# Optimization experiments

Measured on AMD Instinct MI355X. Metric: run time of the kernel, lower is better.

Reference implementation:

```python
import jax, jax.numpy as jnp
import numpy as np

B, H, S, D = 2, 16, 2048, 64

def setup_inputs() -> dict:
    key = jax.random.key(0)
    kq, kk, kv = jax.random.split(key, 3)
    query = jax.random.normal(kq, (B, H, S, D), dtype=jnp.float32)
    key_t = jax.random.normal(kk, (B, H, S, D), dtype=jnp.float32)
    value = jax.random.normal(kv, (B, H, S, D), dtype=jnp.float32)
    # causal mask, broadcast over heads; 0 => masked out
    mask = jnp.tril(jnp.ones((S, S), dtype=jnp.int32))[None, None, :, :]
    mask = jnp.broadcast_to(mask, (B, 1, S, S))
    return {"query": query, "key": key_t, "value": value, "mask": mask}

def reference(query, key, value, mask):
    d_k = query.shape[-1]
    scale = 1.0 / jnp.sqrt(jnp.float32(d_k))
    # [B,H,S,S] scores
    scores = jnp.einsum("bhqd,bhkd->bhqk", query, key) * scale
    scores = jnp.where(mask == 0, jnp.float32(-1e9), scores)
    attn_weights = jax.nn.softmax(scores, axis=-1)
    # dropout is identity in eval mode (reference baseline)
    context = jnp.einsum("bhqk,bhkd->bhqd", attn_weights, value)
    return context, attn_weights
```

## Files before the change

kernel.cpp:

```cpp
#include <hip/hip_runtime.h>

#define S_LEN 2048
#define D_DIM 64
#define BH_N  32
#define QT    64
#define NQT   (S_LEN / QT)
#define SWZ(r) (((r) & 7) << 4)

typedef short bf16x8 __attribute__((ext_vector_type(8)));
typedef float f32x4  __attribute__((ext_vector_type(4)));
typedef unsigned short u16;
typedef unsigned int   u32;

static __device__ __forceinline__ u16 f2bf(float x) {
    unsigned u = __float_as_uint(x);
    u += 0x7fffu + ((u >> 16) & 1u);
    return (u16)(u >> 16);
}
static __device__ __forceinline__ u32 pack2(float a, float b) {
    return (u32)f2bf(a) | ((u32)f2bf(b) << 16);
}

#define MFMA(a, b, acc) __builtin_amdgcn_mfma_f32_16x16x32_bf16((a), (b), (acc), 0, 0, 0)

static __device__ __forceinline__ void gld16(const void* g, void* l) {
    __builtin_amdgcn_global_load_lds((const __attribute__((address_space(1))) void*)g,
                                     (__attribute__((address_space(3))) void*)l, 16, 0, 0);
}

__global__ __launch_bounds__(256)
void build_imgs(const float* __restrict__ K, const float* __restrict__ V,
                u16* __restrict__ Kimg, u16* __restrict__ Vimg)
{
    const int blk = blockIdx.x;
    const int tid = threadIdx.x;
    const float* Ksrc = K + (size_t)blk * 4096;
    const float* Vsrc = V + (size_t)blk * 4096;
    char* Kt = (char*)(Kimg + (size_t)blk * 4096);
    char* Vt = (char*)(Vimg + (size_t)blk * 4096);
    {
        int kr = tid >> 2, kcb = (tid & 3) * 16;
        const float* p = Ksrc + kr * 64 + kcb;
        float4 a = ((const float4*)p)[0], b = ((const float4*)p)[1];
        float4 e = ((const float4*)p)[2], d = ((const float4*)p)[3];
        u32 t[8] = {pack2(a.x,a.y), pack2(a.z,a.w), pack2(b.x,b.y), pack2(b.z,b.w),
                    pack2(e.x,e.y), pack2(e.z,e.w), pack2(d.x,d.y), pack2(d.z,d.w)};
        char* dst = Kt + kr * 128;
        *(uint4*)(dst + ((2*kcb)      ^ SWZ(kr))) = ((uint4*)t)[0];
        *(uint4*)(dst + ((2*kcb + 16) ^ SWZ(kr))) = ((uint4*)t)[1];
    }
    {
        int vk2 = (tid & 31) * 2, vdh = tid >> 5;
        const float* p0 = Vsrc + vk2 * 64 + vdh * 8;
        const float* p1 = p0 + 64;
        float4 a0 = ((const float4*)p0)[0], b0 = ((const float4*)p0)[1];
        float4 a1 = ((const float4*)p1)[0], b1 = ((const float4*)p1)[1];
        float e0[8] = {a0.x,a0.y,a0.z,a0.w,b0.x,b0.y,b0.z,b0.w};
        float e1[8] = {a1.x,a1.y,a1.z,a1.w,b1.x,b1.y,b1.z,b1.w};
        #pragma unroll
        for (int i = 0; i < 8; ++i) {
            int d = vdh * 8 + i;
            *(u32*)(Vt + d * 128 + ((2 * vk2) ^ SWZ(d))) = pack2(e0[i], e1[i]);
        }
    }
}

__global__ __launch_bounds__(256, 4)
void sdpa_pipe(const float* __restrict__ Qg, const u16* __restrict__ Kimg,
               const u16* __restrict__ Vimg, float* __restrict__ out)
{
    __shared__ __attribute__((aligned(16))) char Ksh[2][8192];
    __shared__ __attribute__((aligned(16))) char Vsh[2][8192];
    __shared__ __attribute__((aligned(16))) char Ps[4 * 2048];

    const int tid  = threadIdx.x;
    const int lane = tid & 63;
    const int w    = tid >> 6;
    const int g    = lane >> 4;
    const int c    = lane & 15;

    const int b  = blockIdx.x;
    const int bh = b & (BH_N - 1);
    const int t  = b >> 5;
    const int ti = t & 7, tj = t >> 3;
    const int qi = (tj == 0) ? ti : (tj == 1) ? (15 - ti) : (tj == 2) ? (16 + ti) : (31 - ti);
    const int q0 = qi * QT;

    const char*  Kt = (const char*)(Kimg + (size_t)bh * 32 * 4096);
    const char*  Vt = (const char*)(Vimg + (size_t)bh * 32 * 4096);
    const float* Qh = Qg + (size_t)bh * S_LEN * D_DIM;
    float* ctx  = out + (size_t)bh * S_LEN * D_DIM;
    float* attn = out + (size_t)BH_N * S_LEN * D_DIM + (size_t)bh * S_LEN * S_LEN;

    const int qrow = q0 + w * 16 + c;

    bf16x8 qf0, qf1;
    {
        const float* qp = Qh + (size_t)qrow * D_DIM;
        #pragma unroll
        for (int h = 0; h < 2; ++h) {
            int d0 = h * 32 + g * 8;
            float4 x = *reinterpret_cast<const float4*>(qp + d0);
            float4 y = *reinterpret_cast<const float4*>(qp + d0 + 4);
            u32 tt[4] = {pack2(x.x,x.y), pack2(x.z,x.w), pack2(y.x,y.y), pack2(y.z,y.w)};
            if (h == 0) qf0 = *reinterpret_cast<bf16x8*>(tt);
            else        qf1 = *reinterpret_cast<bf16x8*>(tt);
        }
    }

    const int swz = SWZ(c);
    int off0[4], off1[4];
    #pragma unroll
    for (int s4 = 0; s4 < 4; ++s4) {
        int base = (s4 * 16 + c) * 128;
        off0[s4] = base + ((16 * g)      ^ swz);
        off1[s4] = base + ((64 + 16 * g) ^ swz);
    }

    const float scale = 0.125f;
    float lsum = 0.f;
    f32x4 ot[4];
    #pragma unroll
    for (int i = 0; i < 4; ++i) ot[i] = (f32x4){0.f, 0.f, 0.f, 0.f};
    char* psw = Ps + w * 2048;

    const int t16 = tid * 16;

    {
        gld16(Kt + t16,        Ksh[0] + t16);
        gld16(Kt + t16 + 4096, Ksh[0] + t16 + 4096);
        gld16(Vt + t16,        Vsh[0] + t16);
        gld16(Vt + t16 + 4096, Vsh[0] + t16 + 4096);
    }
    __syncthreads();

    int cur = 0;
    for (int kt = 0; kt <= qi; ++kt) {
        if (kt < qi) {
            const char* kn = Kt + (size_t)(kt + 1) * 8192;
            const char* vn = Vt + (size_t)(kt + 1) * 8192;
            gld16(kn + t16,        Ksh[cur ^ 1] + t16);
            gld16(kn + t16 + 4096, Ksh[cur ^ 1] + t16 + 4096);
            gld16(vn + t16,        Vsh[cur ^ 1] + t16);
            gld16(vn + t16 + 4096, Vsh[cur ^ 1] + t16 + 4096);
        }

        const char* ktile = Ksh[cur];
        const char* vtile = Vsh[cur];
        #pragma unroll
        for (int ks = 0; ks < 4; ++ks) {
            bf16x8 a0 = *reinterpret_cast<const bf16x8*>(ktile + off0[ks]);
            bf16x8 a1 = *reinterpret_cast<const bf16x8*>(ktile + off1[ks]);
            f32x4 s = (f32x4){0.f, 0.f, 0.f, 0.f};
            s = MFMA(a0, qf0, s);
            s = MFMA(a1, qf1, s);
            int kg0 = kt * 64 + ks * 16 + 4 * g;
            float u[4];
            #pragma unroll
            for (int r = 0; r < 4; ++r) {
                float e = __expf(s[r] * scale);
                u[r] = (kg0 + r > qrow) ? 0.f : e;
                lsum += u[r];
            }
            *reinterpret_cast<uint2*>(psw + c * 128 + 32 * ks + 8 * g) =
                make_uint2(pack2(u[0], u[1]), pack2(u[2], u[3]));
        }
        bf16x8 pb0 = *reinterpret_cast<const bf16x8*>(psw + c * 128 + 16 * g);
        bf16x8 pb1 = *reinterpret_cast<const bf16x8*>(psw + c * 128 + 64 + 16 * g);
        #pragma unroll
        for (int ds = 0; ds < 4; ++ds) {
            bf16x8 va0 = *reinterpret_cast<const bf16x8*>(vtile + off0[ds]);
            bf16x8 va1 = *reinterpret_cast<const bf16x8*>(vtile + off1[ds]);
            ot[ds] = MFMA(va0, pb0, ot[ds]);
            ot[ds] = MFMA(va1, pb1, ot[ds]);
        }

        __syncthreads();
        cur ^= 1;
    }

    lsum += __shfl_xor(lsum, 16);
    lsum += __shfl_xor(lsum, 32);
    const float linv = 1.0f / lsum;

    #pragma unroll
    for (int ds = 0; ds < 4; ++ds) {
        f32x4 v = ot[ds] * linv;
        *reinterpret_cast<f32x4*>(ctx + (size_t)qrow * D_DIM + ds * 16 + 4 * g) = v;
    }

    {
        gld16(Kt + t16,        Ksh[0] + t16);
        gld16(Kt + t16 + 4096, Ksh[0] + t16 + 4096);
    }
    __syncthreads();

    cur = 0;
    for (int kt = 0; kt <= qi; ++kt) {
        if (kt < qi) {
            const char* kn = Kt + (size_t)(kt + 1) * 8192;
            gld16(kn + t16,        Ksh[cur ^ 1] + t16);
            gld16(kn + t16 + 4096, Ksh[cur ^ 1] + t16 + 4096);
        }
        const char* ktile = Ksh[cur];
        #pragma unroll
        for (int ks = 0; ks < 4; ++ks) {
            bf16x8 a0 = *reinterpret_cast<const bf16x8*>(ktile + off0[ks]);
            bf16x8 a1 = *reinterpret_cast<const bf16x8*>(ktile + off1[ks]);
            f32x4 s = (f32x4){0.f, 0.f, 0.f, 0.f};
            s = MFMA(a0, qf0, s);
            s = MFMA(a1, qf1, s);
            int kg0 = kt * 64 + ks * 16 + 4 * g;
            f32x4 uu;
            #pragma unroll
            for (int r = 0; r < 4; ++r) {
                float e = __expf(s[r] * scale) * linv;
                uu[r] = (kg0 + r > qrow) ? 0.f : e;
            }
            *reinterpret_cast<f32x4*>(attn + (size_t)qrow * S_LEN + kg0) = uu;
        }
        __syncthreads();
        cur ^= 1;
    }

    const int c40 = ((qi + 1) * QT) >> 2;
    for (int r = w; r < QT; r += 4) {
        float4* rp = reinterpret_cast<float4*>(attn + (size_t)(q0 + r) * S_LEN);
        for (int c4 = c40 + lane; c4 < (S_LEN >> 2); c4 += 64)
            rp[c4] = make_float4(0.f, 0.f, 0.f, 0.f);
    }
}

static __device__ __forceinline__ void stage_k(const float* __restrict__ Kh, int kt,
                                               u16* __restrict__ Ks, int kr, int kcb) {
    const float* kp = Kh + (size_t)(kt * QT + kr) * D_DIM + kcb;
    float4 a = *reinterpret_cast<const float4*>(kp + 0);
    float4 b = *reinterpret_cast<const float4*>(kp + 4);
    float4 e = *reinterpret_cast<const float4*>(kp + 8);
    float4 d = *reinterpret_cast<const float4*>(kp + 12);
    u16 t16[16] = {f2bf(a.x), f2bf(a.y), f2bf(a.z), f2bf(a.w),
                   f2bf(b.x), f2bf(b.y), f2bf(b.z), f2bf(b.w),
                   f2bf(e.x), f2bf(e.y), f2bf(e.z), f2bf(e.w),
                   f2bf(d.x), f2bf(d.y), f2bf(d.z), f2bf(d.w)};
    char* dst = (char*)Ks + kr * 128;
    *reinterpret_cast<uint4*>(dst + ((2 * kcb)      ^ SWZ(kr))) = reinterpret_cast<uint4*>(t16)[0];
    *reinterpret_cast<uint4*>(dst + ((2 * kcb + 16) ^ SWZ(kr))) = reinterpret_cast<uint4*>(t16)[1];
}

__global__ __launch_bounds__(256)
void sdpa_tq(const float* __restrict__ Qg, const float* __restrict__ Kg,
             const float* __restrict__ Vg, float* __restrict__ out)
{
    __shared__ __attribute__((aligned(16))) u16 Ks[QT * D_DIM];
    __shared__ __attribute__((aligned(16))) u16 Vts[D_DIM * QT];
    __shared__ __attribute__((aligned(16))) u16 Psf[4 * 16 * D_DIM];

    const int tid  = threadIdx.x;
    const int lane = tid & 63;
    const int w    = tid >> 6;
    const int g    = lane >> 4;
    const int c    = lane & 15;
    const int b  = blockIdx.x;
    const int bh = b & (BH_N - 1);
    const int qi = (NQT - 1) - (b >> 5);
    const int q0 = qi * QT;

    const size_t hoff = (size_t)bh * S_LEN * D_DIM;
    const float* Qh = Qg + hoff;
    const float* Kh = Kg + hoff;
    const float* Vh = Vg + hoff;
    float* ctx  = out + hoff;
    float* attn = out + (size_t)BH_N * S_LEN * D_DIM + (size_t)bh * S_LEN * S_LEN;
    const int qrow = q0 + w * 16 + c;

    bf16x8 qf[2];
    {
        const float* qp = Qh + (size_t)qrow * D_DIM;
        #pragma unroll
        for (int h = 0; h < 2; ++h) {
            int d0 = h * 32 + g * 8;
            float4 x = *reinterpret_cast<const float4*>(qp + d0);
            float4 y = *reinterpret_cast<const float4*>(qp + d0 + 4);
            u16 t8[8] = {f2bf(x.x), f2bf(x.y), f2bf(x.z), f2bf(x.w),
                         f2bf(y.x), f2bf(y.y), f2bf(y.z), f2bf(y.w)};
            qf[h] = *reinterpret_cast<bf16x8*>(t8);
        }
    }

    const int kr  = tid >> 2;
    const int kcb = (tid & 3) * 16;
    const int vk2 = (tid & 31) * 2;
    const int vdh = tid >> 5;

    const float scale = 0.125f;
    float lsum = 0.0f;
    f32x4 ot[4];
    #pragma unroll
    for (int i = 0; i < 4; ++i) ot[i] = (f32x4){0.f, 0.f, 0.f, 0.f};
    char* psw = (char*)Psf + w * 2048;

    for (int kt = 0; kt <= qi; ++kt) {
        __syncthreads();
        stage_k(Kh, kt, Ks, kr, kcb);
        {
            const float* vp0 = Vh + (size_t)(kt * QT + vk2) * D_DIM + vdh * 8;
            const float* vp1 = vp0 + D_DIM;
            float4 a0 = *reinterpret_cast<const float4*>(vp0);
            float4 b0 = *reinterpret_cast<const float4*>(vp0 + 4);
            float4 a1 = *reinterpret_cast<const float4*>(vp1);
            float4 b1 = *reinterpret_cast<const float4*>(vp1 + 4);
            float e0[8] = {a0.x, a0.y, a0.z, a0.w, b0.x, b0.y, b0.z, b0.w};
            float e1[8] = {a1.x, a1.y, a1.z, a1.w, b1.x, b1.y, b1.z, b1.w};
            #pragma unroll
            for (int i = 0; i < 8; ++i) {
                int d = vdh * 8 + i;
                *reinterpret_cast<unsigned*>((char*)Vts + d * 128 + ((2 * vk2) ^ SWZ(d))) =
                    (unsigned)f2bf(e0[i]) | ((unsigned)f2bf(e1[i]) << 16);
            }
        }
        __syncthreads();

        #pragma unroll
        for (int ks = 0; ks < 4; ++ks) {
            int krow = ks * 16 + c;
            const char* kb = (const char*)Ks + krow * 128;
            bf16x8 ka0 = *reinterpret_cast<const bf16x8*>(kb + ((16 * g)      ^ SWZ(krow)));
            bf16x8 ka1 = *reinterpret_cast<const bf16x8*>(kb + ((64 + 16 * g) ^ SWZ(krow)));
            f32x4 s = (f32x4){0.f, 0.f, 0.f, 0.f};
            s = MFMA(ka0, qf[0], s);
            s = MFMA(ka1, qf[1], s);
            int kg0 = kt * QT + ks * 16 + 4 * g;
            u16 up[4];
            #pragma unroll
            for (int r = 0; r < 4; ++r) {
                float u = __expf(s[r] * scale);
                if (kg0 + r > qrow) u = 0.f;
                lsum += u;
                up[r] = f2bf(u);
            }
            *reinterpret_cast<uint2*>(psw + c * 128 + ((2 * (ks * 16 + 4 * g)) ^ SWZ(c))) =
                *reinterpret_cast<uint2*>(up);
        }
        bf16x8 pb0 = *reinterpret_cast<const bf16x8*>(psw + c * 128 + ((16 * g)      ^ SWZ(c)));
        bf16x8 pb1 = *reinterpret_cast<const bf16x8*>(psw + c * 128 + ((64 + 16 * g) ^ SWZ(c)));
        #pragma unroll
        for (int ds = 0; ds < 4; ++ds) {
            int vrow = ds * 16 + c;
            const char* vb = (const char*)Vts + vrow * 128;
            bf16x8 va0 = *reinterpret_cast<const bf16x8*>(vb + ((16 * g)      ^ SWZ(vrow)));
            bf16x8 va1 = *reinterpret_cast<const bf16x8*>(vb + ((64 + 16 * g) ^ SWZ(vrow)));
            ot[ds] = MFMA(va0, pb0, ot[ds]);
            ot[ds] = MFMA(va1, pb1, ot[ds]);
        }
    }

    lsum += __shfl_xor(lsum, 16);
    lsum += __shfl_xor(lsum, 32);
    const float linv = 1.0f / lsum;

    #pragma unroll
    for (int ds = 0; ds < 4; ++ds) {
        f32x4 v = ot[ds] * linv;
        *reinterpret_cast<f32x4*>(ctx + (size_t)qrow * D_DIM + ds * 16 + 4 * g) = v;
    }

    for (int kt = 0; kt <= qi; ++kt) {
        __syncthreads();
        stage_k(Kh, kt, Ks, kr, kcb);
        __syncthreads();
        #pragma unroll
        for (int ks = 0; ks < 4; ++ks) {
            int krow = ks * 16 + c;
            const char* kb = (const char*)Ks + krow * 128;
            bf16x8 ka0 = *reinterpret_cast<const bf16x8*>(kb + ((16 * g)      ^ SWZ(krow)));
            bf16x8 ka1 = *reinterpret_cast<const bf16x8*>(kb + ((64 + 16 * g) ^ SWZ(krow)));
            f32x4 s = (f32x4){0.f, 0.f, 0.f, 0.f};
            s = MFMA(ka0, qf[0], s);
            s = MFMA(ka1, qf[1], s);
            int kg0 = kt * QT + ks * 16 + 4 * g;
            f32x4 uu;
            #pragma unroll
            for (int r = 0; r < 4; ++r) {
                float u = __expf(s[r] * scale) * linv;
                if (kg0 + r > qrow) u = 0.f;
                uu[r] = u;
            }
            *reinterpret_cast<f32x4*>(attn + (size_t)qrow * S_LEN + kg0) = uu;
        }
    }

    const int c40 = ((qi + 1) * QT) >> 2;
    for (int r = w; r < QT; r += 4) {
        float4* rp = reinterpret_cast<float4*>(attn + (size_t)(q0 + r) * S_LEN);
        for (int c4 = c40 + lane; c4 < (S_LEN >> 2); c4 += 64)
            rp[c4] = make_float4(0.f, 0.f, 0.f, 0.f);
    }
}

extern "C" void kernel_launch(void* const* d_in, const int* in_sizes, int n_in,
                              void* d_out, int out_size, void* d_ws, size_t ws_size,
                              hipStream_t stream)
{
    const float* Q = (const float*)d_in[0];
    const float* K = (const float*)d_in[1];
    const float* V = (const float*)d_in[2];
    float* out = (float*)d_out;

    const size_t elems = (size_t)BH_N * S_LEN * D_DIM;
    const size_t need  = elems * 2 * sizeof(u16);

    if (ws_size >= need) {
        u16* Kimg = (u16*)d_ws;
        u16* Vimg = Kimg + elems;
        hipLaunchKernelGGL(build_imgs, dim3(BH_N * 32), dim3(256), 0, stream, K, V, Kimg, Vimg);
        hipLaunchKernelGGL(sdpa_pipe, dim3(BH_N * NQT), dim3(256), 0, stream,
                           Q, (const u16*)Kimg, (const u16*)Vimg, out);
    } else {
        hipLaunchKernelGGL(sdpa_tq, dim3(BH_N * NQT), dim3(256), 0, stream, Q, K, V, out);
    }
}
```

Measured before the change: 156.4 us.

## Use 128-row query tiles with 512-thread blocks and register-staged K/V prefetch

Doubles the query tile per block to 128 rows using 8 waves, so each K/V tile staged in LDS is shared by twice as many query rows. The grid is halved and the causal tile ordering simplified to pair short and long tiles. The async global_load_lds copies are replaced by loads into registers, which are written to LDS after the compute of the current tile. This trades more registers and more threads per block for fewer K/V reloads, and may lower occupancy or change how well load latency is hidden.

```diff
diff --git a/kernel.cpp b/kernel.cpp
--- a/kernel.cpp
+++ b/kernel.cpp
@@ -3,8 +3,8 @@
 #define S_LEN 2048
 #define D_DIM 64
 #define BH_N  32
-#define QT    64
-#define NQT   (S_LEN / QT)
+#define QR    128
+#define KT    64
 #define SWZ(r) (((r) & 7) << 4)
 
 typedef short bf16x8 __attribute__((ext_vector_type(8)));
@@ -22,11 +22,6 @@
 }
 
 #define MFMA(a, b, acc) __builtin_amdgcn_mfma_f32_16x16x32_bf16((a), (b), (acc), 0, 0, 0)
-
-static __device__ __forceinline__ void gld16(const void* g, void* l) {
-    __builtin_amdgcn_global_load_lds((const __attribute__((address_space(1))) void*)g,
-                                     (__attribute__((address_space(3))) void*)l, 16, 0, 0);
-}
 
 __global__ __launch_bounds__(256)
 void build_imgs(const float* __restrict__ K, const float* __restrict__ V,
@@ -65,13 +60,13 @@
     }
 }
 
-__global__ __launch_bounds__(256, 4)
+__global__ __launch_bounds__(512, 4)
 void sdpa_pipe(const float* __restrict__ Qg, const u16* __restrict__ Kimg,
                const u16* __restrict__ Vimg, float* __restrict__ out)
 {
     __shared__ __attribute__((aligned(16))) char Ksh[2][8192];
     __shared__ __attribute__((aligned(16))) char Vsh[2][8192];
-    __shared__ __attribute__((aligned(16))) char Ps[4 * 2048];
+    __shared__ __attribute__((aligned(16))) char Ps[8 * 2048];
 
     const int tid  = threadIdx.x;
     const int lane = tid & 63;
@@ -83,8 +78,9 @@
     const int bh = b & (BH_N - 1);
     const int t  = b >> 5;
     const int ti = t & 7, tj = t >> 3;
-    const int qi = (tj == 0) ? ti : (tj == 1) ? (15 - ti) : (tj == 2) ? (16 + ti) : (31 - ti);
-    const int q0 = qi * QT;
+    const int qi = tj ? (15 - ti) : ti;
+    const int q0 = qi * QR;
+    const int ktend = 2 * qi + 1;
 
     const char*  Kt = (const char*)(Kimg + (size_t)bh * 32 * 4096);
     const char*  Vt = (const char*)(Vimg + (size_t)bh * 32 * 4096);
@@ -125,24 +121,21 @@
     char* psw = Ps + w * 2048;
 
     const int t16 = tid * 16;
-
-    {
-        gld16(Kt + t16,        Ksh[0] + t16);
-        gld16(Kt + t16 + 4096, Ksh[0] + t16 + 4096);
-        gld16(Vt + t16,        Vsh[0] + t16);
-        gld16(Vt + t16 + 4096, Vsh[0] + t16 + 4096);
+    uint4 kpr, vpr;
+
+    {
+        kpr = ((const uint4*)Kt)[tid];
+        vpr = ((const uint4*)Vt)[tid];
+        *(uint4*)(Ksh[0] + t16) = kpr;
+        *(uint4*)(Vsh[0] + t16) = vpr;
     }
     __syncthreads();
 
     int cur = 0;
-    for (int kt = 0; kt <= qi; ++kt) {
-        if (kt < qi) {
-            const char* kn = Kt + (size_t)(kt + 1) * 8192;
-            const char* vn = Vt + (size_t)(kt + 1) * 8192;
-            gld16(kn + t16,        Ksh[cur ^ 1] + t16);
-            gld16(kn + t16 + 4096, Ksh[cur ^ 1] + t16 + 4096);
-            gld16(vn + t16,        Vsh[cur ^ 1] + t16);
-            gld16(vn + t16 + 4096, Vsh[cur ^ 1] + t16 + 4096);
+    for (int kt = 0; kt <= ktend; ++kt) {
+        if (kt < ktend) {
+            kpr = *(const uint4*)(Kt + (size_t)(kt + 1) * 8192 + t16);
+            vpr = *(const uint4*)(Vt + (size_t)(kt + 1) * 8192 + t16);
         }
 
         const char* ktile = Ksh[cur];
@@ -154,7 +147,7 @@
             f32x4 s = (f32x4){0.f, 0.f, 0.f, 0.f};
             s = MFMA(a0, qf0, s);
             s = MFMA(a1, qf1, s);
-            int kg0 = kt * 64 + ks * 16 + 4 * g;
+            int kg0 = kt * KT + ks * 16 + 4 * g;
             float u[4];
             #pragma unroll
             for (int r = 0; r < 4; ++r) {
@@ -175,6 +168,10 @@
             ot[ds] = MFMA(va1, pb1, ot[ds]);
         }
 
+        if (kt < ktend) {
+            *(uint4*)(Ksh[cur ^ 1] + t16) = kpr;
+            *(uint4*)(Vsh[cur ^ 1] + t16) = vpr;
+        }
         __syncthreads();
         cur ^= 1;
     }
@@ -190,17 +187,15 @@
     }
 
     {
-        gld16(Kt + t16,        Ksh[0] + t16);
-        gld16(Kt + t16 + 4096, Ksh[0] + t16 + 4096);
+        kpr = ((const uint4*)Kt)[tid];
+        *(uint4*)(Ksh[0] + t16) = kpr;
     }
     __syncthreads();
 
     cur = 0;
-    for (int kt = 0; kt <= qi; ++kt) {
-        if (kt < qi) {
-            const char* kn = Kt + (size_t)(kt + 1) * 8192;
-            gld16(kn + t16,        Ksh[cur ^ 1] + t16);
-            gld16(kn + t16 + 4096, Ksh[cur ^ 1] + t16 + 4096);
+    for (int kt = 0; kt <= ktend; ++kt) {
+        if (kt < ktend) {
+            kpr = *(const uint4*)(Kt + (size_t)(kt + 1) * 8192 + t16);
         }
         const char* ktile = Ksh[cur];
         #pragma unroll
@@ -210,7 +205,7 @@
             f32x4 s = (f32x4){0.f, 0.f, 0.f, 0.f};
             s = MFMA(a0, qf0, s);
             s = MFMA(a1, qf1, s);
-            int kg0 = kt * 64 + ks * 16 + 4 * g;
+            int kg0 = kt * KT + ks * 16 + 4 * g;
             f32x4 uu;
             #pragma unroll
             for (int r = 0; r < 4; ++r) {
@@ -219,21 +214,27 @@
             }
             *reinterpret_cast<f32x4*>(attn + (size_t)qrow * S_LEN + kg0) = uu;
         }
+        if (kt < ktend) {
+            *(uint4*)(Ksh[cur ^ 1] + t16) = kpr;
+        }
         __syncthreads();
         cur ^= 1;
     }
 
-    const int c40 = ((qi + 1) * QT) >> 2;
-    for (int r = w; r < QT; r += 4) {
+    const int c40 = ((ktend + 1) * KT) >> 2;
+    for (int r = w; r < QR; r += 8) {
         float4* rp = reinterpret_cast<float4*>(attn + (size_t)(q0 + r) * S_LEN);
         for (int c4 = c40 + lane; c4 < (S_LEN >> 2); c4 += 64)
             rp[c4] = make_float4(0.f, 0.f, 0.f, 0.f);
     }
 }
 
+#define FQT 64
+#define FNQT (S_LEN / FQT)
+
 static __device__ __forceinline__ void stage_k(const float* __restrict__ Kh, int kt,
                                                u16* __restrict__ Ks, int kr, int kcb) {
-    const float* kp = Kh + (size_t)(kt * QT + kr) * D_DIM + kcb;
+    const float* kp = Kh + (size_t)(kt * FQT + kr) * D_DIM + kcb;
     float4 a = *reinterpret_cast<const float4*>(kp + 0);
     float4 b = *reinterpret_cast<const float4*>(kp + 4);
     float4 e = *reinterpret_cast<const float4*>(kp + 8);
@@ -251,8 +252,8 @@
 void sdpa_tq(const float* __restrict__ Qg, const float* __restrict__ Kg,
              const float* __restrict__ Vg, float* __restrict__ out)
 {
-    __shared__ __attribute__((aligned(16))) u16 Ks[QT * D_DIM];
-    __shared__ __attribute__((aligned(16))) u16 Vts[D_DIM * QT];
+    __shared__ __attribute__((aligned(16))) u16 Ks[FQT * D_DIM];
+    __shared__ __attribute__((aligned(16))) u16 Vts[D_DIM * FQT];
     __shared__ __attribute__((aligned(16))) u16 Psf[4 * 16 * D_DIM];
 
     const int tid  = threadIdx.x;
@@ -262,8 +263,8 @@
     const int c    = lane & 15;
     const int b  = blockIdx.x;
     const int bh = b & (BH_N - 1);
-    const int qi = (NQT - 1) - (b >> 5);
-    const int q0 = qi * QT;
+    const int qi = (FNQT - 1) - (b >> 5);
+    const int q0 = qi * FQT;
 
     const size_t hoff = (size_t)bh * S_LEN * D_DIM;
     const float* Qh = Qg + hoff;
@@ -303,7 +304,7 @@
         __syncthreads();
         stage_k(Kh, kt, Ks, kr, kcb);
         {
-            const float* vp0 = Vh + (size_t)(kt * QT + vk2) * D_DIM + vdh * 8;
+            const float* vp0 = Vh + (size_t)(kt * FQT + vk2) * D_DIM + vdh * 8;
             const float* vp1 = vp0 + D_DIM;
             float4 a0 = *reinterpret_cast<const float4*>(vp0);
             float4 b0 = *reinterpret_cast<const float4*>(vp0 + 4);
@@ -329,7 +330,7 @@
             f32x4 s = (f32x4){0.f, 0.f, 0.f, 0.f};
             s = MFMA(ka0, qf[0], s);
             s = MFMA(ka1, qf[1], s);
-            int kg0 = kt * QT + ks * 16 + 4 * g;
+            int kg0 = kt * FQT + ks * 16 + 4 * g;
             u16 up[4];
             #pragma unroll
             for (int r = 0; r < 4; ++r) {
@@ -377,7 +378,7 @@
             f32x4 s = (f32x4){0.f, 0.f, 0.f, 0.f};
             s = MFMA(ka0, qf[0], s);
             s = MFMA(ka1, qf[1], s);
-            int kg0 = kt * QT + ks * 16 + 4 * g;
+            int kg0 = kt * FQT + ks * 16 + 4 * g;
             f32x4 uu;
             #pragma unroll
             for (int r = 0; r < 4; ++r) {
@@ -389,8 +390,8 @@
         }
     }
 
-    const int c40 = ((qi + 1) * QT) >> 2;
-    for (int r = w; r < QT; r += 4) {
+    const int c40 = ((qi + 1) * FQT) >> 2;
+    for (int r = w; r < FQT; r += 4) {
         float4* rp = reinterpret_cast<float4*>(attn + (size_t)(q0 + r) * S_LEN);
         for (int c4 = c40 + lane; c4 < (S_LEN >> 2); c4 += 64)
             rp[c4] = make_float4(0.f, 0.f, 0.f, 0.f);
@@ -413,9 +414,9 @@
         u16* Kimg = (u16*)d_ws;
         u16* Vimg = Kimg + elems;
         hipLaunchKernelGGL(build_imgs, dim3(BH_N * 32), dim3(256), 0, stream, K, V, Kimg, Vimg);
-        hipLaunchKernelGGL(sdpa_pipe, dim3(BH_N * NQT), dim3(256), 0, stream,
+        hipLaunchKernelGGL(sdpa_pipe, dim3(BH_N * (S_LEN / QR)), dim3(512), 0, stream,
                            Q, (const u16*)Kimg, (const u16*)Vimg, out);
     } else {
-        hipLaunchKernelGGL(sdpa_tq, dim3(BH_N * NQT), dim3(256), 0, stream, Q, K, V, out);
-    }
-}
+        hipLaunchKernelGGL(sdpa_tq, dim3(BH_N * FNQT), dim3(256), 0, stream, Q, K, V, out);
+    }
+}
```

Result: slower. 169.6 us (+8.4%).
